# Kernel optimization log

Hardware: AMD Instinct MI355X
Metric: run time of the kernel (lower is better)

Reference implementation:

```python
import jax, jax.numpy as jnp
import numpy as np

N_HEADS = 16
N_EMB = 1024
HEAD_SIZE = 64
BLOCK_SIZE = 2048


def setup_inputs() -> dict:
    key = jax.random.key(0)
    k1, k2, k3, k4, k5 = jax.random.split(key, 5)
    B, T, E, H, D = 4, BLOCK_SIZE, N_EMB, N_HEADS, HEAD_SIZE
    s = 1.0 / np.sqrt(E)
    x = jax.random.normal(k1, (B, T, E), dtype=jnp.float32)
    # Stacked per-head projection weights (Linear with bias=False): [H, E, D]
    Wq = jax.random.normal(k2, (H, E, D), dtype=jnp.float32) * s
    Wk = jax.random.normal(k3, (H, E, D), dtype=jnp.float32) * s
    Wv = jax.random.normal(k4, (H, E, D), dtype=jnp.float32) * s
    Wo = jax.random.normal(k5, (H * D, E), dtype=jnp.float32) * (1.0 / np.sqrt(H * D))
    return {"x": x, "Wq": Wq, "Wk": Wk, "Wv": Wv, "Wo": Wo}


def reference(x, Wq, Wk, Wv, Wo):
    # x: [B,T,E]; Wq/Wk/Wv: [H,E,D]; Wo: [H*D,E]
    B, T, E = x.shape
    H, _, D = Wq.shape
    q = jnp.einsum('bte,hed->bhtd', x, Wq)
    k = jnp.einsum('bte,hed->bhtd', x, Wk)
    v = jnp.einsum('bte,hed->bhtd', x, Wv)
    scores = jnp.einsum('bhtd,bhsd->bhts', q, k) * (D ** -0.5)  # [B,H,T,T]
    causal = jnp.tril(jnp.ones((T, T), dtype=bool))
    scores = jnp.where(causal, scores, -jnp.inf)
    wei = jax.nn.softmax(scores, axis=-1)  # dropout is identity in eval mode
    out = jnp.einsum('bhts,bhsd->bhtd', wei, v)  # [B,H,T,D]
    out = out.transpose(0, 2, 1, 3).reshape(B, T, H * D)  # concat heads
    return out @ Wo  # [B,T,E]
```

## Files before the change

### kernel.cpp

```cpp
#include <hip/hip_runtime.h>

#define B_  4
#define T_  2048
#define E_  1024
#define H_  16
#define D_  64
#define HD_ 1024
#define BT_ 8192

typedef __bf16 bf16x8 __attribute__((ext_vector_type(8)));
typedef float  f32x4  __attribute__((ext_vector_type(4)));

static __device__ __forceinline__ unsigned short f2bf(float f) {
  __bf16 h = (__bf16)f;
  return __builtin_bit_cast(unsigned short, h);
}
static __device__ __forceinline__ bf16x8 ldb8(const unsigned short* p) {
  return *(const bf16x8*)p;
}

#define GLD_LDS16(gp, lp)                                                      \
  __builtin_amdgcn_global_load_lds(                                            \
      (const __attribute__((address_space(1))) void*)(gp),                     \
      (__attribute__((address_space(3))) void*)(lp), 16, 0, 0)


__global__ __launch_bounds__(256) void cast_x_k(const float* __restrict__ x,
                                                unsigned short* __restrict__ xb) {
  int i = blockIdx.x * 256 + threadIdx.x;
  float4 v = ((const float4*)x)[i];
  ushort4 o;
  o.x = f2bf(v.x); o.y = f2bf(v.y); o.z = f2bf(v.z); o.w = f2bf(v.w);
  ((ushort4*)xb)[i] = o;
}

__global__ __launch_bounds__(256) void cast_wqkv_k(const float* __restrict__ Wq,
                                                   const float* __restrict__ Wk,
                                                   const float* __restrict__ Wv,
                                                   unsigned short* __restrict__ wT) {
  int tid = blockIdx.x * 256 + threadIdx.x;
  int e = tid & (E_ - 1);
  int d = (tid >> 10) & (D_ - 1);
  int h = (tid >> 16) & (H_ - 1);
  int w = tid >> 20;
  const float* src = (w == 0) ? Wq : (w == 1) ? Wk : Wv;
  wT[tid] = f2bf(src[(h * E_ + e) * D_ + d]);
}

__global__ __launch_bounds__(256) void cast_wo_k(const float* __restrict__ Wo,
                                                 unsigned short* __restrict__ woT) {
  int tid = blockIdx.x * 256 + threadIdx.x;
  int hd = tid & (HD_ - 1);
  int e  = tid >> 10;
  woT[tid] = f2bf(Wo[hd * E_ + e]);
}

static __device__ __forceinline__ void gemm_core(const unsigned short* __restrict__ A,
                                                 const unsigned short* __restrict__ BT,
                                                 const int K, const int m0, const int n0,
                                                 unsigned short* lA, unsigned short* lB,
                                                 f32x4 acc[4][4]) {
  const int tid  = threadIdx.x;
  const int wave = tid >> 6;
  const int lane = tid & 63;
  const int wm = wave & 1, wn = wave >> 1;
  const int l16 = lane & 15, quad = lane >> 4;

  const unsigned short* gA = A + (size_t)(m0 + (tid >> 2)) * K + (tid & 3) * 8;
  const unsigned short* gB = BT + (size_t)(n0 + (tid >> 2)) * K + (tid & 3) * 8;

  #pragma unroll
  for (int i = 0; i < 4; ++i)
    #pragma unroll
    for (int j = 0; j < 4; ++j) acc[i][j] = (f32x4){0.f, 0.f, 0.f, 0.f};

  const int nit = K >> 5;
  GLD_LDS16(gA, lA + wave * 512);
  GLD_LDS16(gA + (size_t)64 * K, lA + 2048 + wave * 512);
  GLD_LDS16(gB, lB + wave * 512);
  GLD_LDS16(gB + (size_t)64 * K, lB + 2048 + wave * 512);

  for (int it = 0; it < nit; ++it) {
    __syncthreads();
    if (it + 1 < nit) {
      const int kb = (it + 1) * 32;
      const int nb = ((it + 1) & 1) * 4096;
      GLD_LDS16(gA + kb, lA + nb + wave * 512);
      GLD_LDS16(gA + (size_t)64 * K + kb, lA + nb + 2048 + wave * 512);
      GLD_LDS16(gB + kb, lB + nb + wave * 512);
      GLD_LDS16(gB + (size_t)64 * K + kb, lB + nb + 2048 + wave * 512);
    }
    const unsigned short* cA = lA + (it & 1) * 4096;
    const unsigned short* cB = lB + (it & 1) * 4096;
    bf16x8 aF[4], bF[4];
    #pragma unroll
    for (int i = 0; i < 4; ++i)
      aF[i] = ldb8(cA + (wm * 64 + i * 16 + l16) * 32 + quad * 8);
    #pragma unroll
    for (int j = 0; j < 4; ++j)
      bF[j] = ldb8(cB + (wn * 64 + j * 16 + l16) * 32 + quad * 8);
    #pragma unroll
    for (int i = 0; i < 4; ++i)
      #pragma unroll
      for (int j = 0; j < 4; ++j)
        acc[i][j] = __builtin_amdgcn_mfma_f32_16x16x32_bf16(aF[i], bF[j], acc[i][j], 0, 0, 0);
  }
}

__global__ __launch_bounds__(256) void qkv_gemm_k(const unsigned short* __restrict__ xb,
                                                  const unsigned short* __restrict__ wT,
                                                  unsigned short* __restrict__ q,
                                                  unsigned short* __restrict__ k,
                                                  unsigned short* __restrict__ vT) {
  __shared__ unsigned short lA[2 * 128 * 32], lB[2 * 128 * 32];
  f32x4 acc[4][4];
  const int m0 = blockIdx.x * 128, n0 = blockIdx.y * 128;
  gemm_core(xb, wT, E_, m0, n0, lA, lB, acc);

  const int wave = threadIdx.x >> 6, lane = threadIdx.x & 63;
  const int wm = wave & 1, wn = wave >> 1;
  const int l16 = lane & 15, quad = lane >> 4;
  const int type = n0 >> 10;
  const float C = 0.18033688011112042f;
  #pragma unroll
  for (int i = 0; i < 4; ++i) {
    #pragma unroll
    for (int j = 0; j < 4; ++j) {
      const int n = n0 + wn * 64 + j * 16 + l16;
      const int h = (n >> 6) & 15, d = n & 63;
      #pragma unroll
      for (int r = 0; r < 4; ++r) {
        const int m = m0 + wm * 64 + i * 16 + quad * 4 + r;
        const int b = m >> 11, t = m & (T_ - 1);
        if (type == 0)
          q[((size_t)(b * H_ + h) * T_ + t) * D_ + d] = f2bf(acc[i][j][r] * C);
        else if (type == 1)
          k[((size_t)(b * H_ + h) * T_ + t) * D_ + d] = f2bf(acc[i][j][r]);
        else
          vT[((size_t)(b * H_ + h) * D_ + d) * T_ + t] = f2bf(acc[i][j][r]);
      }
    }
  }
}

__global__ __launch_bounds__(256) void proj_k(const unsigned short* __restrict__ ao,
                                              const unsigned short* __restrict__ woT,
                                              float* __restrict__ out) {
  __shared__ unsigned short lA[2 * 128 * 32], lB[2 * 128 * 32];
  f32x4 acc[4][4];
  const int m0 = blockIdx.x * 128, n0 = blockIdx.y * 128;
  gemm_core(ao, woT, HD_, m0, n0, lA, lB, acc);

  const int wave = threadIdx.x >> 6, lane = threadIdx.x & 63;
  const int wm = wave & 1, wn = wave >> 1;
  const int l16 = lane & 15, quad = lane >> 4;
  #pragma unroll
  for (int i = 0; i < 4; ++i)
    #pragma unroll
    for (int j = 0; j < 4; ++j)
      #pragma unroll
      for (int r = 0; r < 4; ++r)
        out[(size_t)(m0 + wm * 64 + i * 16 + quad * 4 + r) * E_ +
            n0 + wn * 64 + j * 16 + l16] = acc[i][j][r];
}

__global__ __launch_bounds__(256) void attn_k(const unsigned short* __restrict__ q,
                                              const unsigned short* __restrict__ k,
                                              const unsigned short* __restrict__ vT,
                                              unsigned short* __restrict__ ao) {
  __shared__ unsigned short lK[2][64 * 64];
  __shared__ unsigned short lV[2][64 * 64];
  __shared__ unsigned short lP[4][32][72];
  const int tid  = threadIdx.x;
  const int lane = tid & 63;
  const int wave = tid >> 6;
  const int l16  = lane & 15;
  const int quad = lane >> 4;
  const int id    = (int)blockIdx.x;
  const int bhid  = id & 63;
  const int qpair = id >> 6;
  const int h = bhid & 15, b = bhid >> 4;
  const size_t bh = (size_t)(b * H_ + h);
  const unsigned short* qp = q  + bh * (T_ * D_);
  const unsigned short* kp = k  + bh * (T_ * D_);
  const unsigned short* vp = vT + bh * (D_ * T_);

  const int srow = tid >> 3;
  const int kseg = (tid & 7) ^ (srow & 7);
  const int sw = (l16 & 7);

  #pragma unroll
  for (int pr = 0; pr < 2; ++pr) {
    const int qblk = (pr == 0) ? qpair : 15 - qpair;
    const int q0 = qblk * 128 + wave * 32;

    bf16x8 aq[2][2];
    #pragma unroll
    for (int rb = 0; rb < 2; ++rb)
      #pragma unroll
      for (int hh = 0; hh < 2; ++hh)
        aq[rb][hh] = ldb8(qp + (q0 + rb * 16 + l16) * D_ + hh * 32 + quad * 8);

    float lr[2][4];
    f32x4 o[2][4];
    #pragma unroll
    for (int rb = 0; rb < 2; ++rb) {
      #pragma unroll
      for (int r = 0; r < 4; ++r) lr[rb][r] = 0.f;
      #pragma unroll
      for (int nb = 0; nb < 4; ++nb) o[rb][nb] = (f32x4){0.f, 0.f, 0.f, 0.f};
    }

    const int nch = 2 * (qblk + 1);

    {
      unsigned short* Kb = lK[0];
      unsigned short* Vb = lV[0];
      GLD_LDS16(kp + srow * D_ + kseg * 8, Kb + wave * 512);
      GLD_LDS16(kp + (32 + srow) * D_ + kseg * 8, Kb + 2048 + wave * 512);
      GLD_LDS16(vp + (size_t)srow * T_ + kseg * 8, Vb + wave * 512);
      GLD_LDS16(vp + (size_t)(32 + srow) * T_ + kseg * 8, Vb + 2048 + wave * 512);
    }

    for (int c = 0; c < nch; ++c) {
      __syncthreads();
      if (c + 1 < nch) {
        const int s1 = (c + 1) * 64;
        unsigned short* Kb = lK[(c + 1) & 1];
        unsigned short* Vb = lV[(c + 1) & 1];
        GLD_LDS16(kp + (s1 + srow) * D_ + kseg * 8, Kb + wave * 512);
        GLD_LDS16(kp + (s1 + 32 + srow) * D_ + kseg * 8, Kb + 2048 + wave * 512);
        GLD_LDS16(vp + (size_t)srow * T_ + s1 + kseg * 8, Vb + wave * 512);
        GLD_LDS16(vp + (size_t)(32 + srow) * T_ + s1 + kseg * 8, Vb + 2048 + wave * 512);
      }
      const int s0 = c * 64;
      const unsigned short* Kb = lK[c & 1];
      const unsigned short* Vb = lV[c & 1];
      f32x4 sc[2][4];
      #pragma unroll
      for (int rb = 0; rb < 2; ++rb)
        #pragma unroll
        for (int j = 0; j < 4; ++j) sc[rb][j] = (f32x4){0.f, 0.f, 0.f, 0.f};
      #pragma unroll
      for (int j = 0; j < 4; ++j) {
        const int sr = j * 16 + l16;
        bf16x8 bk0 = ldb8(Kb + sr * 64 + ((quad ^ sw) << 3));
        bf16x8 bk1 = ldb8(Kb + sr * 64 + (((4 + quad) ^ sw) << 3));
        #pragma unroll
        for (int rb = 0; rb < 2; ++rb) {
          sc[rb][j] = __builtin_amdgcn_mfma_f32_16x16x32_bf16(aq[rb][0], bk0, sc[rb][j], 0, 0, 0);
          sc[rb][j] = __builtin_amdgcn_mfma_f32_16x16x32_bf16(aq[rb][1], bk1, sc[rb][j], 0, 0, 0);
        }
      }
      const bool domask = (c == nch - 1) || (c == nch - 2);
      #pragma unroll
      for (int rb = 0; rb < 2; ++rb) {
        #pragma unroll
        for (int j = 0; j < 4; ++j) {
          #pragma unroll
          for (int r = 0; r < 4; ++r) {
            float p = __builtin_amdgcn_exp2f(sc[rb][j][r]);
            if (domask) {
              const int qg = q0 + rb * 16 + quad * 4 + r;
              if (s0 + j * 16 + l16 > qg) p = 0.f;
            }
            lr[rb][r] += p;
            lP[wave][rb * 16 + quad * 4 + r][j * 16 + l16] = f2bf(p);
          }
        }
      }
      __builtin_amdgcn_wave_barrier();
      bf16x8 aP[2][2];
      #pragma unroll
      for (int rb = 0; rb < 2; ++rb)
        #pragma unroll
        for (int hh = 0; hh < 2; ++hh)
          aP[rb][hh] = ldb8(&lP[wave][rb * 16 + l16][hh * 32 + quad * 8]);
      __builtin_amdgcn_wave_barrier();
      #pragma unroll
      for (int nb = 0; nb < 4; ++nb) {
        const int d = nb * 16 + l16;
        bf16x8 bV0 = ldb8(Vb + d * 64 + ((quad ^ sw) << 3));
        bf16x8 bV1 = ldb8(Vb + d * 64 + (((4 + quad) ^ sw) << 3));
        #pragma unroll
        for (int rb = 0; rb < 2; ++rb) {
          o[rb][nb] = __builtin_amdgcn_mfma_f32_16x16x32_bf16(aP[rb][0], bV0, o[rb][nb], 0, 0, 0);
          o[rb][nb] = __builtin_amdgcn_mfma_f32_16x16x32_bf16(aP[rb][1], bV1, o[rb][nb], 0, 0, 0);
        }
      }
    }

    #pragma unroll
    for (int off = 1; off < 16; off <<= 1)
      #pragma unroll
      for (int rb = 0; rb < 2; ++rb)
        #pragma unroll
        for (int r = 0; r < 4; ++r)
          lr[rb][r] += __shfl_xor(lr[rb][r], off, 64);
    #pragma unroll
    for (int rb = 0; rb < 2; ++rb) {
      #pragma unroll
      for (int r = 0; r < 4; ++r) {
        const float inv = 1.0f / lr[rb][r];
        const int t = q0 + rb * 16 + quad * 4 + r;
        #pragma unroll
        for (int nb = 0; nb < 4; ++nb)
          ao[((size_t)(b * T_ + t) * H_ + h) * D_ + nb * 16 + l16] = f2bf(o[rb][nb][r] * inv);
      }
    }
  }
}


extern "C" void kernel_launch(void* const* d_in, const int* in_sizes, int n_in,
                              void* d_out, int out_size, void* d_ws, size_t ws_size,
                              hipStream_t stream) {
  const float* x  = (const float*)d_in[0];
  const float* Wq = (const float*)d_in[1];
  const float* Wk = (const float*)d_in[2];
  const float* Wv = (const float*)d_in[3];
  const float* Wo = (const float*)d_in[4];
  float* out = (float*)d_out;

  char* ws = (char*)d_ws;
  unsigned short* xb   = (unsigned short*)(ws + 0);
  unsigned short* wT   = (unsigned short*)(ws + 16777216);
  unsigned short* woT  = (unsigned short*)(ws + 23068672);
  unsigned short* qb   = (unsigned short*)(ws + 25165824);
  unsigned short* kb   = (unsigned short*)(ws + 41943040);
  unsigned short* vTb  = (unsigned short*)(ws + 58720256);
  unsigned short* aob  = (unsigned short*)(ws + 75497472);

  cast_x_k<<<dim3((BT_ * E_) / 4 / 256), dim3(256), 0, stream>>>(x, xb);
  cast_wqkv_k<<<dim3((3 * H_ * D_ * E_) / 256), dim3(256), 0, stream>>>(Wq, Wk, Wv, wT);
  cast_wo_k<<<dim3((E_ * HD_) / 256), dim3(256), 0, stream>>>(Wo, woT);
  qkv_gemm_k<<<dim3(BT_ / 128, 3072 / 128), dim3(256), 0, stream>>>(xb, wT, qb, kb, vTb);
  attn_k<<<dim3(512), dim3(256), 0, stream>>>(qb, kb, vTb, aob);
  proj_k<<<dim3(BT_ / 128, E_ / 128), dim3(256), 0, stream>>>(aob, woT, out);
}
```

Before: 283.1 us.

## Triple-buffer GEMM LDS pipeline with XOR swizzle and MFMA priority

The shared GEMM core used by the QKV and output-projection kernels moves from double to triple buffering. Loads are issued two iterations ahead, and explicit vmcnt waits plus a raw barrier replace the per-iteration __syncthreads. Global-to-LDS writes and LDS fragment reads use an XOR swizzle on the 16-byte slot index to reduce bank conflicts, and the MFMA block runs at raised wave priority. This hides more global-load latency at the cost of 50% more LDS per block, which could lower occupancy. The attention kernel is not changed.

Measured after the change: 278.7 us. Within noise of the previous version (-1.6%).

```diff
diff --git a/kernel.cpp b/kernel.cpp
--- a/kernel.cpp
+++ b/kernel.cpp
@@ -66,8 +66,13 @@
   const int wm = wave & 1, wn = wave >> 1;
   const int l16 = lane & 15, quad = lane >> 4;
 
-  const unsigned short* gA = A + (size_t)(m0 + (tid >> 2)) * K + (tid & 3) * 8;
-  const unsigned short* gB = BT + (size_t)(n0 + (tid >> 2)) * K + (tid & 3) * 8;
+  const int srow = tid >> 2;
+  const int sq   = (tid & 3) ^ (srow & 3);
+  const unsigned short* gA = A + (size_t)(m0 + srow) * K + sq * 8;
+  const unsigned short* gB = BT + (size_t)(n0 + srow) * K + sq * 8;
+
+  const int sk = l16 & 3;
+  const int slot0 = (quad ^ sk) << 3;
 
   #pragma unroll
   for (int i = 0; i < 4; ++i)
@@ -79,31 +84,48 @@
   GLD_LDS16(gA + (size_t)64 * K, lA + 2048 + wave * 512);
   GLD_LDS16(gB, lB + wave * 512);
   GLD_LDS16(gB + (size_t)64 * K, lB + 2048 + wave * 512);
-
+  GLD_LDS16(gA + 32, lA + 4096 + wave * 512);
+  GLD_LDS16(gA + (size_t)64 * K + 32, lA + 4096 + 2048 + wave * 512);
+  GLD_LDS16(gB + 32, lB + 4096 + wave * 512);
+  GLD_LDS16(gB + (size_t)64 * K + 32, lB + 4096 + 2048 + wave * 512);
+  asm volatile("s_waitcnt vmcnt(4)" ::: "memory");
+  __builtin_amdgcn_s_barrier();
+
+  int cb = 0, sb = 2;
   for (int it = 0; it < nit; ++it) {
-    __syncthreads();
-    if (it + 1 < nit) {
-      const int kb = (it + 1) * 32;
-      const int nb = ((it + 1) & 1) * 4096;
-      GLD_LDS16(gA + kb, lA + nb + wave * 512);
-      GLD_LDS16(gA + (size_t)64 * K + kb, lA + nb + 2048 + wave * 512);
-      GLD_LDS16(gB + kb, lB + nb + wave * 512);
-      GLD_LDS16(gB + (size_t)64 * K + kb, lB + nb + 2048 + wave * 512);
-    }
-    const unsigned short* cA = lA + (it & 1) * 4096;
-    const unsigned short* cB = lB + (it & 1) * 4096;
+    if (it + 2 < nit) {
+      const int kb = (it + 2) * 32;
+      const int so = sb * 4096;
+      GLD_LDS16(gA + kb, lA + so + wave * 512);
+      GLD_LDS16(gA + (size_t)64 * K + kb, lA + so + 2048 + wave * 512);
+      GLD_LDS16(gB + kb, lB + so + wave * 512);
+      GLD_LDS16(gB + (size_t)64 * K + kb, lB + so + 2048 + wave * 512);
+    }
+    const unsigned short* cA = lA + cb * 4096;
+    const unsigned short* cB = lB + cb * 4096;
     bf16x8 aF[4], bF[4];
     #pragma unroll
     for (int i = 0; i < 4; ++i)
-      aF[i] = ldb8(cA + (wm * 64 + i * 16 + l16) * 32 + quad * 8);
+      aF[i] = ldb8(cA + (wm * 64 + i * 16 + l16) * 32 + slot0);
     #pragma unroll
     for (int j = 0; j < 4; ++j)
-      bF[j] = ldb8(cB + (wn * 64 + j * 16 + l16) * 32 + quad * 8);
+      bF[j] = ldb8(cB + (wn * 64 + j * 16 + l16) * 32 + slot0);
+    __builtin_amdgcn_s_setprio(1);
     #pragma unroll
     for (int i = 0; i < 4; ++i)
       #pragma unroll
       for (int j = 0; j < 4; ++j)
         acc[i][j] = __builtin_amdgcn_mfma_f32_16x16x32_bf16(aF[i], bF[j], acc[i][j], 0, 0, 0);
+    __builtin_amdgcn_s_setprio(0);
+    if (it + 1 < nit) {
+      if (it + 2 < nit)
+        asm volatile("s_waitcnt vmcnt(4)" ::: "memory");
+      else
+        asm volatile("s_waitcnt vmcnt(0)" ::: "memory");
+      __builtin_amdgcn_s_barrier();
+    }
+    cb = (cb == 2) ? 0 : cb + 1;
+    sb = (sb == 2) ? 0 : sb + 1;
   }
 }
 
@@ -112,7 +134,7 @@
                                                   unsigned short* __restrict__ q,
                                                   unsigned short* __restrict__ k,
                                                   unsigned short* __restrict__ vT) {
-  __shared__ unsigned short lA[2 * 128 * 32], lB[2 * 128 * 32];
+  __shared__ unsigned short lA[3 * 128 * 32], lB[3 * 128 * 32];
   f32x4 acc[4][4];
   const int m0 = blockIdx.x * 128, n0 = blockIdx.y * 128;
   gemm_core(xb, wT, E_, m0, n0, lA, lB, acc);
@@ -146,7 +168,7 @@
 __global__ __launch_bounds__(256) void proj_k(const unsigned short* __restrict__ ao,
                                               const unsigned short* __restrict__ woT,
                                               float* __restrict__ out) {
-  __shared__ unsigned short lA[2 * 128 * 32], lB[2 * 128 * 32];
+  __shared__ unsigned short lA[3 * 128 * 32], lB[3 * 128 * 32];
   f32x4 acc[4][4];
   const int m0 = blockIdx.x * 128, n0 = blockIdx.y * 128;
   gemm_core(ao, woT, HD_, m0, n0, lA, lB, acc);
```

## Rewrite GEMM core with 128x256 tiles, 3-stage LDS pipeline and swizzle

Applied to the files above, without the earlier changes.

The shared GEMM core moves from 128x128 tiles with 4 waves and a 2-buffer K=32 loop to 128x256 tiles with 8 waves, K=64 steps, a triple-buffered LDS pipeline driven by explicit vmcnt waits and barriers, XOR-swizzled LDS layout, and s_setprio around the MFMA bursts. Both the QKV and output-projection GEMMs use it, launched as 1D grids with a remapped block order for L2 locality. The aim is fewer LDS bank conflicts, more overlap of global loads with MFMA work, and more reuse per tile. The cost is much more LDS per block (144 KB), which limits occupancy, plus a fragile hand-counted vmcnt schedule.

After: 298.3 us. 1.05x slower.

```diff
diff --git a/kernel.cpp b/kernel.cpp
--- a/kernel.cpp
+++ b/kernel.cpp
@@ -63,62 +63,118 @@
   const int tid  = threadIdx.x;
   const int wave = tid >> 6;
   const int lane = tid & 63;
-  const int wm = wave & 1, wn = wave >> 1;
+  const int wm = wave >> 2, wn = wave & 3;
   const int l16 = lane & 15, quad = lane >> 4;
-
-  const unsigned short* gA = A + (size_t)(m0 + (tid >> 2)) * K + (tid & 3) * 8;
-  const unsigned short* gB = BT + (size_t)(n0 + (tid >> 2)) * K + (tid & 3) * 8;
+  const int nkt = K >> 6;
+
+  const int sr = tid >> 3;
+  const int sc = ((tid & 7) ^ (sr & 7)) * 8;
+
+  const int sw = l16 & 7;
+  const int sl0 = ((quad ^ sw)) << 3;
+  const int sl1 = ((4 + quad) ^ sw) << 3;
+
+#define STAGE_A_(kt, ah)                                                        \
+  GLD_LDS16(A + (size_t)(m0 + (ah) * 64 + sr) * K + (kt) * 64 + sc,             \
+            lA + ((kt) % 3) * 8192 + (ah) * 4096 + wave * 512)
+#define STAGE_B_(kt, bh, ii)                                                    \
+  GLD_LDS16(BT + (size_t)(n0 + (bh) * 128 + (ii) * 64 + sr) * K + (kt) * 64 + sc, \
+            lB + ((kt) % 3) * 16384 + (bh) * 8192 + (ii) * 4096 + wave * 512)
+#define STAGE_KT_A(kt) do { STAGE_A_(kt, 0); STAGE_A_(kt, 1); } while (0)
+#define STAGE_KT_B(kt) do { STAGE_B_(kt, 0, 0); STAGE_B_(kt, 0, 1);             \
+                            STAGE_B_(kt, 1, 0); STAGE_B_(kt, 1, 1); } while (0)
 
   #pragma unroll
   for (int i = 0; i < 4; ++i)
     #pragma unroll
     for (int j = 0; j < 4; ++j) acc[i][j] = (f32x4){0.f, 0.f, 0.f, 0.f};
 
-  const int nit = K >> 5;
-  GLD_LDS16(gA, lA + wave * 512);
-  GLD_LDS16(gA + (size_t)64 * K, lA + 2048 + wave * 512);
-  GLD_LDS16(gB, lB + wave * 512);
-  GLD_LDS16(gB + (size_t)64 * K, lB + 2048 + wave * 512);
-
-  for (int it = 0; it < nit; ++it) {
-    __syncthreads();
-    if (it + 1 < nit) {
-      const int kb = (it + 1) * 32;
-      const int nb = ((it + 1) & 1) * 4096;
-      GLD_LDS16(gA + kb, lA + nb + wave * 512);
-      GLD_LDS16(gA + (size_t)64 * K + kb, lA + nb + 2048 + wave * 512);
-      GLD_LDS16(gB + kb, lB + nb + wave * 512);
-      GLD_LDS16(gB + (size_t)64 * K + kb, lB + nb + 2048 + wave * 512);
-    }
-    const unsigned short* cA = lA + (it & 1) * 4096;
-    const unsigned short* cB = lB + (it & 1) * 4096;
-    bf16x8 aF[4], bF[4];
-    #pragma unroll
-    for (int i = 0; i < 4; ++i)
-      aF[i] = ldb8(cA + (wm * 64 + i * 16 + l16) * 32 + quad * 8);
-    #pragma unroll
-    for (int j = 0; j < 4; ++j)
-      bF[j] = ldb8(cB + (wn * 64 + j * 16 + l16) * 32 + quad * 8);
-    #pragma unroll
-    for (int i = 0; i < 4; ++i)
-      #pragma unroll
-      for (int j = 0; j < 4; ++j)
-        acc[i][j] = __builtin_amdgcn_mfma_f32_16x16x32_bf16(aF[i], bF[j], acc[i][j], 0, 0, 0);
+  STAGE_KT_A(0); STAGE_KT_B(0);
+  STAGE_KT_A(1); STAGE_KT_B(1);
+  STAGE_KT_A(2);
+  asm volatile("s_waitcnt vmcnt(8)" ::: "memory");
+  __builtin_amdgcn_s_barrier();
+
+  for (int kt = 0; kt < nkt; ++kt) {
+    const unsigned short* cA = lA + (kt % 3) * 8192;
+    const unsigned short* cB = lB + (kt % 3) * 16384;
+    bf16x8 aF[4][2], bF[2][2];
+    #pragma unroll
+    for (int mi = 0; mi < 4; ++mi) {
+      const int ar = wm * 64 + mi * 16 + l16;
+      aF[mi][0] = ldb8(cA + ar * 64 + sl0);
+      aF[mi][1] = ldb8(cA + ar * 64 + sl1);
+    }
+    #pragma unroll
+    for (int ni = 0; ni < 2; ++ni) {
+      const int br = wn * 64 + ni * 16 + l16;
+      bF[ni][0] = ldb8(cB + br * 64 + sl0);
+      bF[ni][1] = ldb8(cB + br * 64 + sl1);
+    }
+    if (kt + 2 < nkt) {
+      STAGE_KT_B(kt + 2);
+      asm volatile("s_waitcnt vmcnt(10)" ::: "memory");
+    } else {
+      asm volatile("s_waitcnt vmcnt(0)" ::: "memory");
+    }
+    __builtin_amdgcn_s_barrier();
+    __builtin_amdgcn_s_setprio(1);
+    #pragma unroll
+    for (int mi = 0; mi < 4; ++mi)
+      #pragma unroll
+      for (int ni = 0; ni < 2; ++ni)
+        #pragma unroll
+        for (int ks = 0; ks < 2; ++ks)
+          acc[mi][ni] = __builtin_amdgcn_mfma_f32_16x16x32_bf16(aF[mi][ks], bF[ni][ks],
+                                                                acc[mi][ni], 0, 0, 0);
+    __builtin_amdgcn_s_setprio(0);
+    __builtin_amdgcn_s_barrier();
+    bf16x8 bG[2][2];
+    #pragma unroll
+    for (int ni = 0; ni < 2; ++ni) {
+      const int br = wn * 64 + (2 + ni) * 16 + l16;
+      bG[ni][0] = ldb8(cB + br * 64 + sl0);
+      bG[ni][1] = ldb8(cB + br * 64 + sl1);
+    }
+    if (kt + 3 < nkt) {
+      STAGE_KT_A(kt + 3);
+      asm volatile("s_waitcnt vmcnt(8)" ::: "memory");
+    } else {
+      asm volatile("s_waitcnt vmcnt(0)" ::: "memory");
+    }
+    __builtin_amdgcn_s_barrier();
+    __builtin_amdgcn_s_setprio(1);
+    #pragma unroll
+    for (int mi = 0; mi < 4; ++mi)
+      #pragma unroll
+      for (int ni = 0; ni < 2; ++ni)
+        #pragma unroll
+        for (int ks = 0; ks < 2; ++ks)
+          acc[mi][2 + ni] = __builtin_amdgcn_mfma_f32_16x16x32_bf16(aF[mi][ks], bG[ni][ks],
+                                                                    acc[mi][2 + ni], 0, 0, 0);
+    __builtin_amdgcn_s_setprio(0);
+    __builtin_amdgcn_s_barrier();
   }
-}
-
-__global__ __launch_bounds__(256) void qkv_gemm_k(const unsigned short* __restrict__ xb,
+#undef STAGE_A_
+#undef STAGE_B_
+#undef STAGE_KT_A
+#undef STAGE_KT_B
+}
+
+__global__ __launch_bounds__(512) void qkv_gemm_k(const unsigned short* __restrict__ xb,
                                                   const unsigned short* __restrict__ wT,
                                                   unsigned short* __restrict__ q,
                                                   unsigned short* __restrict__ k,
                                                   unsigned short* __restrict__ vT) {
-  __shared__ unsigned short lA[2 * 128 * 32], lB[2 * 128 * 32];
+  __shared__ unsigned short lA[3 * 8192];
+  __shared__ unsigned short lB[3 * 16384];
   f32x4 acc[4][4];
-  const int m0 = blockIdx.x * 128, n0 = blockIdx.y * 128;
+  const int id = ((int)blockIdx.x & 7) * 96 + ((int)blockIdx.x >> 3);
+  const int m0 = (id & 63) * 128, n0 = (id >> 6) * 256;
   gemm_core(xb, wT, E_, m0, n0, lA, lB, acc);
 
   const int wave = threadIdx.x >> 6, lane = threadIdx.x & 63;
-  const int wm = wave & 1, wn = wave >> 1;
+  const int wm = wave >> 2, wn = wave & 3;
   const int l16 = lane & 15, quad = lane >> 4;
   const int type = n0 >> 10;
   const float C = 0.18033688011112042f;
@@ -143,16 +199,18 @@
   }
 }
 
-__global__ __launch_bounds__(256) void proj_k(const unsigned short* __restrict__ ao,
+__global__ __launch_bounds__(512) void proj_k(const unsigned short* __restrict__ ao,
                                               const unsigned short* __restrict__ woT,
                                               float* __restrict__ out) {
-  __shared__ unsigned short lA[2 * 128 * 32], lB[2 * 128 * 32];
+  __shared__ unsigned short lA[3 * 8192];
+  __shared__ unsigned short lB[3 * 16384];
   f32x4 acc[4][4];
-  const int m0 = blockIdx.x * 128, n0 = blockIdx.y * 128;
+  const int id = ((int)blockIdx.x & 7) * 32 + ((int)blockIdx.x >> 3);
+  const int m0 = (id & 63) * 128, n0 = (id >> 6) * 256;
   gemm_core(ao, woT, HD_, m0, n0, lA, lB, acc);
 
   const int wave = threadIdx.x >> 6, lane = threadIdx.x & 63;
-  const int wm = wave & 1, wn = wave >> 1;
+  const int wm = wave >> 2, wn = wave & 3;
   const int l16 = lane & 15, quad = lane >> 4;
   #pragma unroll
   for (int i = 0; i < 4; ++i)
@@ -334,7 +392,7 @@
   cast_x_k<<<dim3((BT_ * E_) / 4 / 256), dim3(256), 0, stream>>>(x, xb);
   cast_wqkv_k<<<dim3((3 * H_ * D_ * E_) / 256), dim3(256), 0, stream>>>(Wq, Wk, Wv, wT);
   cast_wo_k<<<dim3((E_ * HD_) / 256), dim3(256), 0, stream>>>(Wo, woT);
-  qkv_gemm_k<<<dim3(BT_ / 128, 3072 / 128), dim3(256), 0, stream>>>(xb, wT, qb, kb, vTb);
+  qkv_gemm_k<<<dim3(768), dim3(512), 0, stream>>>(xb, wT, qb, kb, vTb);
   attn_k<<<dim3(512), dim3(256), 0, stream>>>(qb, kb, vTb, aob);
-  proj_k<<<dim3(BT_ / 128, E_ / 128), dim3(256), 0, stream>>>(aob, woT, out);
-}
+  proj_k<<<dim3(256), dim3(512), 0, stream>>>(aob, woT, out);
+}
```
